# Kernel tuning notes

Hardware: AMD Instinct MI355X
Metric: run time of the kernel (lower is better)

Reference implementation:

```python
import jax, jax.numpy as jnp
import numpy as np
from jax import lax

TEMP = 1.0
K_OPS = 8
N_PARAMS = 4

# OP_BANK: each op takes (canvas (H,W) float, p (4,) float) -> new values (H,W).
# The masked merge where(mask, new, canvas) is applied by the caller.

def op_recolor(cv, p):
    return jnp.full_like(cv, p[0])

def op_add(cv, p):
    return cv + p[0]

def op_scale(cv, p):
    return cv * p[1]

def op_affine(cv, p):
    return cv * p[0] + p[1]

def op_blend(cv, p):
    a = jax.nn.sigmoid(p[2])
    return (1.0 - a) * cv + a * p[0]

def op_invert(cv, p):
    return p[0] - cv

def op_tanh_mod(cv, p):
    return jnp.tanh(cv * p[0] + p[1]) * p[2] + p[3]

def op_offset(cv, p):
    return cv + p[0] * p[1]

OPS = [op_recolor, op_add, op_scale, op_affine, op_blend, op_invert, op_tanh_mod, op_offset]


def setup_inputs() -> dict:
    key = jax.random.key(0)
    ks = jax.random.split(key, 8)
    N, D, H, W = 256, 512, 1024, 1024
    canvas = jax.random.uniform(ks[0], (H, W), dtype=jnp.float32) * 9.0  # color-ish values
    attr_tensor = jax.random.normal(ks[1], (N, D), dtype=jnp.float32)
    obj_masks = jax.random.randint(ks[2], (N, H, W), 0, 2) > 0  # bool (N,H,W)
    u = jnp.clip(jax.random.uniform(ks[3], (N, K_OPS), dtype=jnp.float32), 1e-6, 1.0 - 1e-6)
    gumbel = -jnp.log(-jnp.log(u))
    selector_w = jax.random.normal(ks[4], (D, K_OPS), dtype=jnp.float32) * (D ** -0.5)
    selector_b = jnp.zeros((K_OPS,), dtype=jnp.float32)
    param_w = jax.random.normal(ks[5], (D, K_OPS * N_PARAMS), dtype=jnp.float32) * (D ** -0.5)
    param_b = jnp.zeros((K_OPS * N_PARAMS,), dtype=jnp.float32)
    return {"canvas": canvas, "attr_tensor": attr_tensor, "obj_masks": obj_masks,
            "gumbel": gumbel, "selector_w": selector_w, "selector_b": selector_b,
            "param_w": param_w, "param_b": param_b}


def reference(canvas, attr_tensor, obj_masks, gumbel, selector_w, selector_b, param_w, param_b):
    N, D = attr_tensor.shape
    K = selector_b.shape[0]
    # selector logits / temp, then gumbel-softmax hard == argmax(logits/temp + g)
    sel_logits = (attr_tensor @ selector_w + selector_b) / TEMP  # (N,K)
    k_sel = jnp.argmax(sel_logits / TEMP + gumbel, axis=-1)       # (N,) int
    params_raw = (attr_tensor @ param_w + param_b).reshape(N, K, N_PARAMS)
    p_sel = jnp.take_along_axis(params_raw, k_sel[:, None, None], axis=1)[:, 0, :]  # (N,4)

    def step(cv, xs):
        k_i, mask_i, p_i = xs
        new_vals = lax.switch(k_i, OPS, cv, p_i)
        return jnp.where(mask_i, new_vals, cv), None

    canvas, _ = lax.scan(step, canvas, (k_sel, obj_masks, p_sel))
    return canvas
```

## Files before the change

kernel.cpp:

```cpp
#include <hip/hip_runtime.h>
#include <hip/hip_bf16.h>
#include <cmath>

#define HWPX (1024*1024)
#define NOBJ 256
#define DDIM 512

__global__ __launch_bounds__(256) void detect_kernel(const unsigned int* __restrict__ m,
                                                     int* __restrict__ flag) {
    __shared__ int s;
    if (threadIdx.x == 0) s = 0;
    __syncthreads();
    if (m[threadIdx.x] > 1u) atomicOr(&s, 1);
    __syncthreads();
    if (threadIdx.x == 0) *flag = s;
}

__global__ __launch_bounds__(64) void prep_kernel(
    const float* __restrict__ attr,
    const float* __restrict__ selw,
    const float* __restrict__ selb,
    const float* __restrict__ gumbel,
    const float* __restrict__ pw,
    const float* __restrict__ pb,
    float4* __restrict__ coef,
    int* __restrict__ kindArr)
{
    const int n = blockIdx.x;
    const int l = threadIdx.x;

    float a[8];
#pragma unroll
    for (int j = 0; j < 8; ++j) a[j] = attr[n * DDIM + l + 64 * j];

    float best = -1e30f;
    int bestk = 0;
#pragma unroll
    for (int k = 0; k < 8; ++k) {
        float s = 0.f;
#pragma unroll
        for (int j = 0; j < 8; ++j) s += a[j] * selw[(l + 64 * j) * 8 + k];
#pragma unroll
        for (int off = 32; off; off >>= 1) s += __shfl_xor(s, off);
        float v = s + selb[k] + gumbel[n * 8 + k];
        if (v > best) { best = v; bestk = k; }
    }
    bestk = __shfl(bestk, 0);

    float p[4];
#pragma unroll
    for (int qi = 0; qi < 4; ++qi) {
        float s = 0.f;
#pragma unroll
        for (int j = 0; j < 8; ++j) s += a[j] * pw[(l + 64 * j) * 32 + bestk * 4 + qi];
#pragma unroll
        for (int off = 32; off; off >>= 1) s += __shfl_xor(s, off);
        p[qi] = s + pb[bestk * 4 + qi];
    }

    if (l == 0) {
        float A = 1.f, B = 0.f;
        switch (bestk) {
            case 0: A = 0.f;  B = p[0]; break;
            case 1: A = 1.f;  B = p[0]; break;
            case 2: A = p[1]; B = 0.f;  break;
            case 3: A = p[0]; B = p[1]; break;
            case 4: { float aa = 1.f / (1.f + expf(-p[2]));
                      A = 1.f - aa; B = aa * p[0]; } break;
            case 5: A = -1.f; B = p[0]; break;
            case 6: break;
            default: A = 1.f; B = p[0] * p[1]; break;
        }
        if (bestk == 6) {
            coef[n] = make_float4(p[0], p[1], p[2], p[3]);
            kindArr[n] = 6;
        } else {
            coef[n] = make_float4(A, B, 0.f, 0.f);
            kindArr[n] = 0;
        }
    }
}

__global__ __launch_bounds__(256) void apply_kernel(
    const float* __restrict__ canvas,
    const unsigned char* __restrict__ masksB,
    const float4* __restrict__ coef,
    const int* __restrict__ kindArr,
    const int* __restrict__ flagP,
    float* __restrict__ out)
{
    const int tid = blockIdx.x * blockDim.x + threadIdx.x;
    const size_t base = (size_t)tid * 8;

    float c[8];
    {
        const float4* cv = (const float4*)(canvas + base);
        float4 x = cv[0], y = cv[1];
        c[0] = x.x; c[1] = x.y; c[2] = x.z; c[3] = x.w;
        c[4] = y.x; c[5] = y.y; c[6] = y.z; c[7] = y.w;
    }

    const int isBool = __builtin_amdgcn_readfirstlane(*flagP);

    if (isBool) {
        uint2 mn = *(const uint2*)(masksB + base);
        for (int i = 0; i < NOBJ; ++i) {
            uint2 m = mn;
            int nx = (i + 1 < NOBJ) ? (i + 1) : (NOBJ - 1);
            mn = *(const uint2*)(masksB + (size_t)nx * HWPX + base);
            float4 q = coef[i];
            int kd = __builtin_amdgcn_readfirstlane(kindArr[i]);
            if (kd == 6) {
#pragma unroll
                for (int j = 0; j < 8; ++j) {
                    unsigned w = (j < 4) ? m.x : m.y;
                    float e = __expf(2.0f * fmaf(c[j], q.x, q.y));
                    float t = 1.0f - 2.0f / (e + 1.0f);
                    float v = fmaf(t, q.z, q.w);
                    c[j] = ((w >> ((j & 3) * 8)) & 1u) ? v : c[j];
                }
            } else {
#pragma unroll
                for (int j = 0; j < 8; ++j) {
                    unsigned w = (j < 4) ? m.x : m.y;
                    float v = fmaf(c[j], q.x, q.y);
                    c[j] = ((w >> ((j & 3) * 8)) & 1u) ? v : c[j];
                }
            }
        }
    } else {
        const int* mi = (const int*)masksB;
        int4 mn0, mn1;
        { const int4* mp = (const int4*)(mi + base); mn0 = mp[0]; mn1 = mp[1]; }
        for (int i = 0; i < NOBJ; ++i) {
            int4 m0 = mn0, m1 = mn1;
            int nx = (i + 1 < NOBJ) ? (i + 1) : (NOBJ - 1);
            { const int4* mp = (const int4*)(mi + (size_t)nx * HWPX + base);
              mn0 = mp[0]; mn1 = mp[1]; }
            float4 q = coef[i];
            int kd = __builtin_amdgcn_readfirstlane(kindArr[i]);
            int mm[8] = {m0.x, m0.y, m0.z, m0.w, m1.x, m1.y, m1.z, m1.w};
            if (kd == 6) {
#pragma unroll
                for (int j = 0; j < 8; ++j) {
                    float e = __expf(2.0f * fmaf(c[j], q.x, q.y));
                    float t = 1.0f - 2.0f / (e + 1.0f);
                    float v = fmaf(t, q.z, q.w);
                    c[j] = mm[j] ? v : c[j];
                }
            } else {
#pragma unroll
                for (int j = 0; j < 8; ++j) {
                    float v = fmaf(c[j], q.x, q.y);
                    c[j] = mm[j] ? v : c[j];
                }
            }
        }
    }

    {
        float4* ov = (float4*)(out + base);
        ov[0] = make_float4(c[0], c[1], c[2], c[3]);
        ov[1] = make_float4(c[4], c[5], c[6], c[7]);
    }
}

extern "C" void kernel_launch(void* const* d_in, const int* in_sizes, int n_in,
                              void* d_out, int out_size, void* d_ws, size_t ws_size,
                              hipStream_t stream) {
    const float* canvas        = (const float*)d_in[0];
    const float* attr          = (const float*)d_in[1];
    const unsigned char* masks = (const unsigned char*)d_in[2];
    const float* gumbel        = (const float*)d_in[3];
    const float* selw          = (const float*)d_in[4];
    const float* selb          = (const float*)d_in[5];
    const float* pw            = (const float*)d_in[6];
    const float* pb            = (const float*)d_in[7];
    float* out = (float*)d_out;

    float4* coef = (float4*)d_ws;
    int* kindArr = (int*)((char*)d_ws + NOBJ * sizeof(float4));
    int* flag = kindArr + NOBJ;

    detect_kernel<<<1, 256, 0, stream>>>((const unsigned int*)masks, flag);
    prep_kernel<<<NOBJ, 64, 0, stream>>>(attr, selw, selb, gumbel, pw, pb, coef, kindArr);
    apply_kernel<<<HWPX / (256 * 8), 256, 0, stream>>>(canvas, masks, coef, kindArr, flag, out);
}
```

Baseline: 1.334 ms.

## Preload all mask bytes into bitmasks with more threads and LDS coefficients

The apply kernel now handles 2 pixels per thread instead of 8, launching four times as many blocks. Each thread first issues all 256 mask loads (unrolled) and packs them into per-pixel bitmasks, then runs the op chain from registers. Coefficients and op kinds are staged in shared memory. The goal is to expose far more memory-level parallelism on the 256MB mask stream. The cost is narrow 2-byte loads per object, which may reduce coalescing efficiency, and higher register pressure from the unrolled loads.

```diff
diff --git a/kernel.cpp b/kernel.cpp
--- a/kernel.cpp
+++ b/kernel.cpp
@@ -5,6 +5,7 @@
 #define HWPX (1024*1024)
 #define NOBJ 256
 #define DDIM 512
+#define PXT 2
 
 __global__ __launch_bounds__(256) void detect_kernel(const unsigned int* __restrict__ m,
                                                      int* __restrict__ flag) {
@@ -89,80 +90,76 @@
     const int* __restrict__ flagP,
     float* __restrict__ out)
 {
-    const int tid = blockIdx.x * blockDim.x + threadIdx.x;
-    const size_t base = (size_t)tid * 8;
+    __shared__ float4 sCoef[NOBJ];
+    __shared__ int    sKind[NOBJ];
+    const int t = threadIdx.x;
+    sCoef[t] = coef[t];
+    sKind[t] = kindArr[t];
+    __syncthreads();
 
-    float c[8];
-    {
-        const float4* cv = (const float4*)(canvas + base);
-        float4 x = cv[0], y = cv[1];
-        c[0] = x.x; c[1] = x.y; c[2] = x.z; c[3] = x.w;
-        c[4] = y.x; c[5] = y.y; c[6] = y.z; c[7] = y.w;
-    }
+    const size_t base = ((size_t)blockIdx.x * 256 + t) * PXT;
+
+    float2 cv = *(const float2*)(canvas + base);
+    float c0 = cv.x, c1 = cv.y;
+
+    unsigned bits0[8], bits1[8];
 
     const int isBool = __builtin_amdgcn_readfirstlane(*flagP);
 
     if (isBool) {
-        uint2 mn = *(const uint2*)(masksB + base);
-        for (int i = 0; i < NOBJ; ++i) {
-            uint2 m = mn;
-            int nx = (i + 1 < NOBJ) ? (i + 1) : (NOBJ - 1);
-            mn = *(const uint2*)(masksB + (size_t)nx * HWPX + base);
-            float4 q = coef[i];
-            int kd = __builtin_amdgcn_readfirstlane(kindArr[i]);
-            if (kd == 6) {
+        const unsigned char* mp = masksB + base;
 #pragma unroll
-                for (int j = 0; j < 8; ++j) {
-                    unsigned w = (j < 4) ? m.x : m.y;
-                    float e = __expf(2.0f * fmaf(c[j], q.x, q.y));
-                    float t = 1.0f - 2.0f / (e + 1.0f);
-                    float v = fmaf(t, q.z, q.w);
-                    c[j] = ((w >> ((j & 3) * 8)) & 1u) ? v : c[j];
-                }
-            } else {
+        for (int w = 0; w < 8; ++w) {
+            unsigned a0 = 0, a1 = 0;
 #pragma unroll
-                for (int j = 0; j < 8; ++j) {
-                    unsigned w = (j < 4) ? m.x : m.y;
-                    float v = fmaf(c[j], q.x, q.y);
-                    c[j] = ((w >> ((j & 3) * 8)) & 1u) ? v : c[j];
-                }
+            for (int j = 0; j < 32; ++j) {
+                const int i = w * 32 + j;
+                unsigned short m = *(const unsigned short*)(mp + (size_t)i * HWPX);
+                a0 |= (unsigned)((m & 0x00FFu) ? 1u : 0u) << j;
+                a1 |= (unsigned)((m & 0xFF00u) ? 1u : 0u) << j;
             }
+            bits0[w] = a0; bits1[w] = a1;
         }
     } else {
         const int* mi = (const int*)masksB;
-        int4 mn0, mn1;
-        { const int4* mp = (const int4*)(mi + base); mn0 = mp[0]; mn1 = mp[1]; }
-        for (int i = 0; i < NOBJ; ++i) {
-            int4 m0 = mn0, m1 = mn1;
-            int nx = (i + 1 < NOBJ) ? (i + 1) : (NOBJ - 1);
-            { const int4* mp = (const int4*)(mi + (size_t)nx * HWPX + base);
-              mn0 = mp[0]; mn1 = mp[1]; }
-            float4 q = coef[i];
-            int kd = __builtin_amdgcn_readfirstlane(kindArr[i]);
-            int mm[8] = {m0.x, m0.y, m0.z, m0.w, m1.x, m1.y, m1.z, m1.w};
-            if (kd == 6) {
 #pragma unroll
-                for (int j = 0; j < 8; ++j) {
-                    float e = __expf(2.0f * fmaf(c[j], q.x, q.y));
-                    float t = 1.0f - 2.0f / (e + 1.0f);
-                    float v = fmaf(t, q.z, q.w);
-                    c[j] = mm[j] ? v : c[j];
-                }
-            } else {
+        for (int w = 0; w < 8; ++w) {
+            unsigned a0 = 0, a1 = 0;
 #pragma unroll
-                for (int j = 0; j < 8; ++j) {
-                    float v = fmaf(c[j], q.x, q.y);
-                    c[j] = mm[j] ? v : c[j];
-                }
+            for (int j = 0; j < 32; ++j) {
+                const int i = w * 32 + j;
+                int2 m = *(const int2*)(mi + (size_t)i * HWPX + base);
+                a0 |= (m.x ? 1u : 0u) << j;
+                a1 |= (m.y ? 1u : 0u) << j;
             }
+            bits0[w] = a0; bits1[w] = a1;
         }
     }
 
-    {
-        float4* ov = (float4*)(out + base);
-        ov[0] = make_float4(c[0], c[1], c[2], c[3]);
-        ov[1] = make_float4(c[4], c[5], c[6], c[7]);
+#pragma unroll
+    for (int w = 0; w < 8; ++w) {
+        const unsigned b0 = bits0[w], b1 = bits1[w];
+        for (int j = 0; j < 32; ++j) {
+            const int i = w * 32 + j;
+            float4 q = sCoef[i];
+            float v0, v1;
+            if (sKind[i] == 6) {
+                float e0 = __expf(2.0f * fmaf(c0, q.x, q.y));
+                float e1 = __expf(2.0f * fmaf(c1, q.x, q.y));
+                float t0 = 1.0f - 2.0f / (e0 + 1.0f);
+                float t1 = 1.0f - 2.0f / (e1 + 1.0f);
+                v0 = fmaf(t0, q.z, q.w);
+                v1 = fmaf(t1, q.z, q.w);
+            } else {
+                v0 = fmaf(c0, q.x, q.y);
+                v1 = fmaf(c1, q.x, q.y);
+            }
+            c0 = ((b0 >> j) & 1u) ? v0 : c0;
+            c1 = ((b1 >> j) & 1u) ? v1 : c1;
+        }
     }
+
+    *(float2*)(out + base) = make_float2(c0, c1);
 }
 
 extern "C" void kernel_launch(void* const* d_in, const int* in_sizes, int n_in,
@@ -184,5 +181,5 @@
 
     detect_kernel<<<1, 256, 0, stream>>>((const unsigned int*)masks, flag);
     prep_kernel<<<NOBJ, 64, 0, stream>>>(attr, selw, selb, gumbel, pw, pb, coef, kindArr);
-    apply_kernel<<<HWPX / (256 * 8), 256, 0, stream>>>(canvas, masks, coef, kindArr, flag, out);
+    apply_kernel<<<HWPX / (256 * PXT), 256, 0, stream>>>(canvas, masks, coef, kindArr, flag, out);
 }
```

Result: slower. 1.371 ms (+2.8%).
